# Kernel optimization log

Measured on AMD Instinct MI355X. Metric: run time of the kernel, lower is better.

The kernel has to match this reference:

```python
import jax, jax.numpy as jnp
import numpy as np

GDEP = 3      # number of diffusion steps
ALPHA = 0.05  # residual mixing coefficient


def setup_inputs() -> dict:
    key = jax.random.key(0)
    k1, k2, k3, k4 = jax.random.split(key, 4)
    B, C, N, L = 256, 32, 207, 12   # batch, channels, nodes, timesteps
    C_OUT = 32
    x = jax.random.normal(k1, (B, C, N, L), dtype=jnp.float32)
    adj = jax.random.uniform(k2, (N, N), dtype=jnp.float32)
    # mlp = 1x1 Conv2d(c_in, c_out): weight (c_out, c_in), bias (c_out,)
    W = jax.random.normal(k3, (C_OUT, C), dtype=jnp.float32) * 0.05
    b = jax.random.normal(k4, (C_OUT,), dtype=jnp.float32) * 0.05
    return {"x": x, "adj": adj, "W": W, "b": b}


def reference(x, adj, W, b):
    # Row-normalized adjacency with self loops: a = (adj + I) / rowsum
    N = adj.shape[0]
    a = adj + jnp.eye(N, dtype=adj.dtype)
    a = a / a.sum(axis=1, keepdims=True)
    # Iterative diffusion with alpha-residual mix
    h = x
    for _ in range(GDEP):
        # nconv: torch.einsum('ncwl,vw->ncvl', x, A)
        h = ALPHA * x + (1.0 - ALPHA) * jnp.einsum('ncwl,vw->ncvl', h, a)
    # mlp: 1x1 conv over channel dim + bias
    ho = jnp.einsum('ncvl,oc->novl', h, W) + b[None, :, None, None]
    return ho
```

## Files before the change

kernel.cpp:

```cpp
#include <hip/hip_runtime.h>

#define NN 207
#define ALPHA 0.05f
#define BETA  0.95f

typedef __attribute__((ext_vector_type(8))) short bf16x8;
typedef __attribute__((ext_vector_type(4))) float f32x4;

__device__ inline unsigned short f2bf(float f) {
    union { float f; unsigned int u; } v; v.f = f;
    unsigned int u = v.u;
    unsigned int r = (u + 0x7FFFu + ((u >> 16) & 1u)) >> 16;
    return (unsigned short)r;
}

__global__ __launch_bounds__(256) void k_norm(const float* __restrict__ adj,
                                              float* __restrict__ An,
                                              float* __restrict__ M1) {
    int v = blockIdx.x;
    int t = threadIdx.x;
    __shared__ float red[4];
    __shared__ float sinv;
    float s = 0.f;
    if (t < NN) s = adj[v * NN + t];
    s += __shfl_down(s, 32); s += __shfl_down(s, 16); s += __shfl_down(s, 8);
    s += __shfl_down(s, 4);  s += __shfl_down(s, 2);  s += __shfl_down(s, 1);
    if ((t & 63) == 0) red[t >> 6] = s;
    __syncthreads();
    if (t == 0) sinv = 1.0f / (red[0] + red[1] + red[2] + red[3] + 1.0f);
    __syncthreads();
    if (t < NN) {
        float val = (adj[v * NN + t] + (t == v ? 1.f : 0.f)) * sinv;
        An[v * NN + t] = val;
        M1[v * NN + t] = (t == v ? ALPHA : 0.f) + BETA * val;
    }
}

__global__ __launch_bounds__(256) void k_step(const float* __restrict__ A,
                                              const float* __restrict__ X,
                                              float* __restrict__ C) {
    __shared__ float As[32][68];
    __shared__ float Xs[32][68];
    const int t = threadIdx.x;
    const int bi = blockIdx.x;
    const int i0 = (bi >> 2) * 64, j0 = (bi & 3) * 64;
    const int ty = t >> 4, tx = t & 15;
    float acc[4][4] = {{0.f}};
    for (int kt = 0; kt < 7; ++kt) {
        __syncthreads();
        {
            int r = t >> 2, q = t & 3;
            int gi = i0 + r;
            #pragma unroll
            for (int h = 0; h < 2; ++h) {
                #pragma unroll
                for (int e = 0; e < 4; ++e) {
                    int u = kt * 32 + q * 8 + h * 4 + e;
                    float v = 0.f;
                    if (gi < NN && u < NN) v = A[gi * NN + u];
                    As[q * 8 + h * 4 + e][r] = v;
                }
            }
            int kk = t >> 3, p = t & 7;
            int gu = kt * 32 + kk;
            #pragma unroll
            for (int h = 0; h < 2; ++h) {
                #pragma unroll
                for (int e = 0; e < 4; ++e) {
                    int gj = j0 + p * 8 + h * 4 + e;
                    float v = 0.f;
                    if (gu < NN && gj < NN) v = X[gu * NN + gj];
                    Xs[kk][p * 8 + h * 4 + e] = v;
                }
            }
        }
        __syncthreads();
        #pragma unroll 8
        for (int kk = 0; kk < 32; ++kk) {
            float4 a = *(const float4*)&As[kk][ty * 4];
            float4 b = *(const float4*)&Xs[kk][tx * 4];
            const float* ap = &a.x; const float* bp = &b.x;
            #pragma unroll
            for (int ii = 0; ii < 4; ++ii)
                #pragma unroll
                for (int jj = 0; jj < 4; ++jj)
                    acc[ii][jj] = fmaf(ap[ii], bp[jj], acc[ii][jj]);
        }
    }
    #pragma unroll
    for (int ii = 0; ii < 4; ++ii) {
        int gi = i0 + ty * 4 + ii;
        if (gi < NN) {
            #pragma unroll
            for (int jj = 0; jj < 4; ++jj) {
                int gj = j0 + tx * 4 + jj;
                if (gj < NN)
                    C[gi * NN + gj] = (gi == gj ? ALPHA : 0.f) + BETA * acc[ii][jj];
            }
        }
    }
}

__global__ __launch_bounds__(64) void k_pack(const float* __restrict__ P,
                                             uint4* __restrict__ Pbf) {
    int g = blockIdx.x;
    int nt = g / 7, ks = g % 7;
    int lane = threadIdx.x;
    int v = nt * 16 + (lane & 15);
    int wb = ks * 32 + (lane >> 4) * 8;
    unsigned int d[4];
    #pragma unroll
    for (int p = 0; p < 4; ++p) {
        float lo = 0.f, hi = 0.f;
        int w = wb + 2 * p;
        if (v < NN) {
            if (w < NN)     lo = P[v * NN + w];
            if (w + 1 < NN) hi = P[v * NN + w + 1];
        }
        d[p] = (unsigned int)f2bf(lo) | ((unsigned int)f2bf(hi) << 16);
    }
    uint4 o; o.x = d[0]; o.y = d[1]; o.z = d[2]; o.w = d[3];
    Pbf[g * 64 + lane] = o;
}

__global__ __launch_bounds__(512) void k_main(const float* __restrict__ x,
                                              const uint4* __restrict__ Pbf,
                                              const float* __restrict__ Wm,
                                              const float* __restrict__ bias,
                                              float* __restrict__ out) {
    __shared__ __align__(16) char lds[52224];
    unsigned int* afrag = (unsigned int*)lds;
    float* ys = (float*)lds;

    const int n = blockIdx.x;
    const int t = threadIdx.x;
    const int lane = t & 63;
    const int wave = __builtin_amdgcn_readfirstlane(t >> 6);

    f32x4 acc[3][13];
    #pragma unroll
    for (int a = 0; a < 3; ++a)
        #pragma unroll
        for (int bI = 0; bI < 13; ++bI) acc[a][bI] = (f32x4)0.f;

    const float4* x4 = (const float4*)x;

    for (int ks = 0; ks < 7; ++ks) {
        __syncthreads();
        #pragma unroll
        for (int i = 0; i < 3; ++i) {
            int q = t + 512 * i;
            int c = q / 48, r = q % 48;
            int wp = r / 3, lseg = r % 3;
            int w0 = ks * 32 + 2 * wp;
            float4 va = make_float4(0.f, 0.f, 0.f, 0.f), vb = va;
            size_t base = (size_t)(n * 32 + c) * NN;
            if (w0 < NN)     va = x4[(base + w0) * 3 + lseg];
            if (w0 + 1 < NN) vb = x4[(base + w0 + 1) * 3 + lseg];
            int kblk = wp >> 2, dw = wp & 3;
            const float* vap = &va.x; const float* vbp = &vb.x;
            #pragma unroll
            for (int e = 0; e < 4; ++e) {
                int m = c * 12 + lseg * 4 + e;
                unsigned int pk = (unsigned int)f2bf(vap[e])
                                | ((unsigned int)f2bf(vbp[e]) << 16);
                afrag[(m >> 4) * 256 + ((m & 15) + 16 * kblk) * 4 + dw] = pk;
            }
        }
        __syncthreads();
        bf16x8 af[3];
        #pragma unroll
        for (int mt3 = 0; mt3 < 3; ++mt3)
            af[mt3] = ((const bf16x8*)lds)[(wave * 3 + mt3) * 64 + lane];
        #pragma unroll
        for (int nt = 0; nt < 13; ++nt) {
            uint4 braw = Pbf[(nt * 7 + ks) * 64 + lane];
            bf16x8 bf = __builtin_bit_cast(bf16x8, braw);
            #pragma unroll
            for (int mt3 = 0; mt3 < 3; ++mt3)
                acc[mt3][nt] = __builtin_amdgcn_mfma_f32_16x16x32_bf16(
                                   af[mt3], bf, acc[mt3][nt], 0, 0, 0);
        }
    }

    #pragma unroll
    for (int np = 0; np < 7; ++np) {
        __syncthreads();
        #pragma unroll
        for (int tl = 0; tl < 2; ++tl) {
            int nt = np * 2 + tl;
            if (nt < 13) {
                #pragma unroll
                for (int mt3 = 0; mt3 < 3; ++mt3) {
                    int mrow = (wave * 3 + mt3) * 16 + (lane >> 4) * 4;
                    #pragma unroll
                    for (int r = 0; r < 4; ++r)
                        ys[(mrow + r) * 34 + tl * 16 + (lane & 15)] = acc[mt3][nt][r];
                }
            }
        }
        __syncthreads();
        if (t < 384) {
            int tl = t / 192, rr = t % 192;
            int vv = rr / 12, l = rr % 12;
            int v = (np * 2 + tl) * 16 + vv;
            if (v < NN) {
                float y[32];
                #pragma unroll
                for (int c = 0; c < 32; ++c)
                    y[c] = ys[(c * 12 + l) * 34 + tl * 16 + vv];
                size_t ob = (size_t)n * 32 * (NN * 12) + (size_t)v * 12 + l;
                for (int o = 0; o < 32; ++o) {
                    float a = bias[o];
                    #pragma unroll
                    for (int c = 0; c < 32; ++c)
                        a = fmaf(Wm[o * 32 + c], y[c], a);
                    out[ob + (size_t)o * (NN * 12)] = a;
                }
            }
        }
    }
}

extern "C" void kernel_launch(void* const* d_in, const int* in_sizes, int n_in,
                              void* d_out, int out_size, void* d_ws, size_t ws_size,
                              hipStream_t stream) {
    const float* x   = (const float*)d_in[0];
    const float* adj = (const float*)d_in[1];
    const float* W   = (const float*)d_in[2];
    const float* b   = (const float*)d_in[3];
    float* out = (float*)d_out;
    float* ws  = (float*)d_ws;

    float* An  = ws;
    float* M1P = ws + 43008;
    float* M2  = ws + 86016;
    uint4* Pbf = (uint4*)ws;

    k_norm<<<NN, 256, 0, stream>>>(adj, An, M1P);
    k_step<<<16, 256, 0, stream>>>(An, M1P, M2);
    k_step<<<16, 256, 0, stream>>>(An, M2, M1P);
    k_pack<<<91, 64, 0, stream>>>(M1P, Pbf);
    k_main<<<256, 512, 0, stream>>>(x, Pbf, W, b, out);
}
```

Before: 261.4 us.

## Split main kernel across timestep segments, fuse bf16 packing into step kernel

The small adjacency power steps now run on 169 16x16 tiles instead of 16 blocks, and the bf16 packing pass is folded into the second step kernel, which removes one launch. The main kernel now uses 768 blocks, one per batch and 4-timestep segment, with an XCD-aware block-to-batch mapping. Each lane builds its MFMA A fragment straight from global memory, so the LDS staging and its barriers are gone. The catch is that x is reread with strided scalar loads and each block redoes the 1x1 conv epilogue for its own slice.

```diff
diff --git a/kernel.cpp b/kernel.cpp
--- a/kernel.cpp
+++ b/kernel.cpp
@@ -10,8 +10,7 @@
 __device__ inline unsigned short f2bf(float f) {
     union { float f; unsigned int u; } v; v.f = f;
     unsigned int u = v.u;
-    unsigned int r = (u + 0x7FFFu + ((u >> 16) & 1u)) >> 16;
-    return (unsigned short)r;
+    return (unsigned short)((u + 0x7FFFu + ((u >> 16) & 1u)) >> 16);
 }
 
 __global__ __launch_bounds__(256) void k_norm(const float* __restrict__ adj,
@@ -36,187 +35,169 @@
     }
 }
 
-__global__ __launch_bounds__(256) void k_step(const float* __restrict__ A,
-                                              const float* __restrict__ X,
-                                              float* __restrict__ C) {
-    __shared__ float As[32][68];
-    __shared__ float Xs[32][68];
+__global__ __launch_bounds__(256) void k_stepM(const float* __restrict__ A,
+                                               const float* __restrict__ X,
+                                               float* __restrict__ C) {
+    __shared__ float As[16 * 208];
+    __shared__ float Xs[16 * 212];
     const int t = threadIdx.x;
-    const int bi = blockIdx.x;
-    const int i0 = (bi >> 2) * 64, j0 = (bi & 3) * 64;
-    const int ty = t >> 4, tx = t & 15;
-    float acc[4][4] = {{0.f}};
-    for (int kt = 0; kt < 7; ++kt) {
-        __syncthreads();
-        {
-            int r = t >> 2, q = t & 3;
-            int gi = i0 + r;
-            #pragma unroll
-            for (int h = 0; h < 2; ++h) {
-                #pragma unroll
-                for (int e = 0; e < 4; ++e) {
-                    int u = kt * 32 + q * 8 + h * 4 + e;
-                    float v = 0.f;
-                    if (gi < NN && u < NN) v = A[gi * NN + u];
-                    As[q * 8 + h * 4 + e][r] = v;
-                }
-            }
-            int kk = t >> 3, p = t & 7;
-            int gu = kt * 32 + kk;
-            #pragma unroll
-            for (int h = 0; h < 2; ++h) {
-                #pragma unroll
-                for (int e = 0; e < 4; ++e) {
-                    int gj = j0 + p * 8 + h * 4 + e;
-                    float v = 0.f;
-                    if (gu < NN && gj < NN) v = X[gu * NN + gj];
-                    Xs[kk][p * 8 + h * 4 + e] = v;
-                }
-            }
-        }
-        __syncthreads();
-        #pragma unroll 8
-        for (int kk = 0; kk < 32; ++kk) {
-            float4 a = *(const float4*)&As[kk][ty * 4];
-            float4 b = *(const float4*)&Xs[kk][tx * 4];
-            const float* ap = &a.x; const float* bp = &b.x;
-            #pragma unroll
-            for (int ii = 0; ii < 4; ++ii)
-                #pragma unroll
-                for (int jj = 0; jj < 4; ++jj)
-                    acc[ii][jj] = fmaf(ap[ii], bp[jj], acc[ii][jj]);
-        }
-    }
-    #pragma unroll
-    for (int ii = 0; ii < 4; ++ii) {
-        int gi = i0 + ty * 4 + ii;
-        if (gi < NN) {
-            #pragma unroll
-            for (int jj = 0; jj < 4; ++jj) {
-                int gj = j0 + tx * 4 + jj;
-                if (gj < NN)
-                    C[gi * NN + gj] = (gi == gj ? ALPHA : 0.f) + BETA * acc[ii][jj];
-            }
-        }
-    }
-}
-
-__global__ __launch_bounds__(64) void k_pack(const float* __restrict__ P,
-                                             uint4* __restrict__ Pbf) {
-    int g = blockIdx.x;
-    int nt = g / 7, ks = g % 7;
-    int lane = threadIdx.x;
-    int v = nt * 16 + (lane & 15);
-    int wb = ks * 32 + (lane >> 4) * 8;
-    unsigned int d[4];
-    #pragma unroll
-    for (int p = 0; p < 4; ++p) {
-        float lo = 0.f, hi = 0.f;
-        int w = wb + 2 * p;
-        if (v < NN) {
-            if (w < NN)     lo = P[v * NN + w];
-            if (w + 1 < NN) hi = P[v * NN + w + 1];
-        }
-        d[p] = (unsigned int)f2bf(lo) | ((unsigned int)f2bf(hi) << 16);
-    }
-    uint4 o; o.x = d[0]; o.y = d[1]; o.z = d[2]; o.w = d[3];
-    Pbf[g * 64 + lane] = o;
-}
-
-__global__ __launch_bounds__(512) void k_main(const float* __restrict__ x,
-                                              const uint4* __restrict__ Pbf,
-                                              const float* __restrict__ Wm,
-                                              const float* __restrict__ bias,
-                                              float* __restrict__ out) {
-    __shared__ __align__(16) char lds[52224];
-    unsigned int* afrag = (unsigned int*)lds;
-    float* ys = (float*)lds;
-
-    const int n = blockIdx.x;
+    const int i0 = (blockIdx.x / 13) * 16, j0 = (blockIdx.x % 13) * 16;
+    const int r = t >> 4, cj = t & 15;
+    for (int p = 0; p < 13; ++p) {
+        int u = p * 16 + cj;
+        As[r * 208 + u] = (i0 + r < NN && u < NN) ? A[(i0 + r) * NN + u] : 0.f;
+        int u2 = p * 16 + r;
+        Xs[cj * 212 + u2] = (u2 < NN && j0 + cj < NN) ? X[u2 * NN + j0 + cj] : 0.f;
+    }
+    __syncthreads();
+    float s = 0.f;
+    for (int u = 0; u < 208; u += 4) {
+        float4 av = *(const float4*)&As[r * 208 + u];
+        float4 xv = *(const float4*)&Xs[cj * 212 + u];
+        s = fmaf(av.x, xv.x, s); s = fmaf(av.y, xv.y, s);
+        s = fmaf(av.z, xv.z, s); s = fmaf(av.w, xv.w, s);
+    }
+    int gi = i0 + r, gj = j0 + cj;
+    if (gi < NN && gj < NN)
+        C[gi * NN + gj] = (gi == gj ? ALPHA : 0.f) + BETA * s;
+}
+
+__global__ __launch_bounds__(256) void k_stepP(const float* __restrict__ A,
+                                               const float* __restrict__ X,
+                                               uint4* __restrict__ Pbf) {
+    __shared__ float As[16 * 208];
+    __shared__ float Xs[16 * 212];
+    __shared__ float Ct[16 * 17];
+    const int t = threadIdx.x;
+    const int nt = blockIdx.x / 13, jt = blockIdx.x % 13;
+    const int i0 = nt * 16, j0 = jt * 16;
+    const int r = t >> 4, cj = t & 15;
+    for (int p = 0; p < 13; ++p) {
+        int u = p * 16 + cj;
+        As[r * 208 + u] = (i0 + r < NN && u < NN) ? A[(i0 + r) * NN + u] : 0.f;
+        int u2 = p * 16 + r;
+        Xs[cj * 212 + u2] = (u2 < NN && j0 + cj < NN) ? X[u2 * NN + j0 + cj] : 0.f;
+    }
+    __syncthreads();
+    float s = 0.f;
+    for (int u = 0; u < 208; u += 4) {
+        float4 av = *(const float4*)&As[r * 208 + u];
+        float4 xv = *(const float4*)&Xs[cj * 212 + u];
+        s = fmaf(av.x, xv.x, s); s = fmaf(av.y, xv.y, s);
+        s = fmaf(av.z, xv.z, s); s = fmaf(av.w, xv.w, s);
+    }
+    int gi = i0 + r, gj = j0 + cj;
+    Ct[r * 17 + cj] = ((gi == gj && gi < NN) ? ALPHA : 0.f) + BETA * s;
+    __syncthreads();
+    if (t < 32) {
+        const int vv = t & 15, kb2 = t >> 4;
+        const int ks = jt >> 1;
+        const int kblk = (jt & 1) * 2 + kb2;
+        unsigned int d[4];
+        #pragma unroll
+        for (int p = 0; p < 4; ++p) {
+            float lo = Ct[vv * 17 + kb2 * 8 + 2 * p];
+            float hi = Ct[vv * 17 + kb2 * 8 + 2 * p + 1];
+            d[p] = (unsigned int)f2bf(lo) | ((unsigned int)f2bf(hi) << 16);
+        }
+        uint4 o; o.x = d[0]; o.y = d[1]; o.z = d[2]; o.w = d[3];
+        Pbf[(nt * 7 + ks) * 64 + vv + 16 * kblk] = o;
+        if (jt == 12) {
+            uint4 z; z.x = z.y = z.z = z.w = 0u;
+            Pbf[(nt * 7 + 6) * 64 + vv + 16 * (2 + kb2)] = z;
+        }
+    }
+}
+
+__global__ __launch_bounds__(512, 4) void k_main(const float* __restrict__ x,
+                                                 const uint4* __restrict__ Pbf,
+                                                 const float* __restrict__ Wm,
+                                                 const float* __restrict__ bias,
+                                                 float* __restrict__ out) {
+    __shared__ float ys[128 * 33];
+
+    const int b = blockIdx.x;
+    const int xcd = b & 7;
+    const int q = b >> 3;
+    const int lseg = q % 3;
+    const int n = (q / 3) * 8 + xcd;
+    const int l0 = lseg * 4;
+
     const int t = threadIdx.x;
     const int lane = t & 63;
     const int wave = __builtin_amdgcn_readfirstlane(t >> 6);
 
-    f32x4 acc[3][13];
+    const int c    = wave * 4 + ((lane >> 2) & 3);
+    const int dl   = lane & 3;
+    const int kblk = lane >> 4;
+    const float* xp = x + ((size_t)(n * 32 + c) * NN + kblk * 8) * 12 + l0 + dl;
+
+    f32x4 acc[13];
     #pragma unroll
-    for (int a = 0; a < 3; ++a)
-        #pragma unroll
-        for (int bI = 0; bI < 13; ++bI) acc[a][bI] = (f32x4)0.f;
-
-    const float4* x4 = (const float4*)x;
+    for (int i = 0; i < 13; ++i) acc[i] = (f32x4)0.f;
 
     for (int ks = 0; ks < 7; ++ks) {
-        __syncthreads();
-        #pragma unroll
-        for (int i = 0; i < 3; ++i) {
-            int q = t + 512 * i;
-            int c = q / 48, r = q % 48;
-            int wp = r / 3, lseg = r % 3;
-            int w0 = ks * 32 + 2 * wp;
-            float4 va = make_float4(0.f, 0.f, 0.f, 0.f), vb = va;
-            size_t base = (size_t)(n * 32 + c) * NN;
-            if (w0 < NN)     va = x4[(base + w0) * 3 + lseg];
-            if (w0 + 1 < NN) vb = x4[(base + w0 + 1) * 3 + lseg];
-            int kblk = wp >> 2, dw = wp & 3;
-            const float* vap = &va.x; const float* vbp = &vb.x;
-            #pragma unroll
-            for (int e = 0; e < 4; ++e) {
-                int m = c * 12 + lseg * 4 + e;
-                unsigned int pk = (unsigned int)f2bf(vap[e])
-                                | ((unsigned int)f2bf(vbp[e]) << 16);
-                afrag[(m >> 4) * 256 + ((m & 15) + 16 * kblk) * 4 + dw] = pk;
+        const float* xk = xp + ks * (32 * 12);
+        float xv[8];
+        if (ks < 6) {
+            #pragma unroll
+            for (int j = 0; j < 8; ++j) xv[j] = xk[j * 12];
+        } else {
+            #pragma unroll
+            for (int j = 0; j < 8; ++j) {
+                int w = 192 + kblk * 8 + j;
+                xv[j] = (w < NN) ? xk[j * 12] : 0.f;
             }
         }
-        __syncthreads();
-        bf16x8 af[3];
-        #pragma unroll
-        for (int mt3 = 0; mt3 < 3; ++mt3)
-            af[mt3] = ((const bf16x8*)lds)[(wave * 3 + mt3) * 64 + lane];
+        uint4 araw;
+        araw.x = (unsigned int)f2bf(xv[0]) | ((unsigned int)f2bf(xv[1]) << 16);
+        araw.y = (unsigned int)f2bf(xv[2]) | ((unsigned int)f2bf(xv[3]) << 16);
+        araw.z = (unsigned int)f2bf(xv[4]) | ((unsigned int)f2bf(xv[5]) << 16);
+        araw.w = (unsigned int)f2bf(xv[6]) | ((unsigned int)f2bf(xv[7]) << 16);
+        bf16x8 af = __builtin_bit_cast(bf16x8, araw);
+
+        const uint4* pb = Pbf + ks * 64 + lane;
         #pragma unroll
         for (int nt = 0; nt < 13; ++nt) {
-            uint4 braw = Pbf[(nt * 7 + ks) * 64 + lane];
-            bf16x8 bf = __builtin_bit_cast(bf16x8, braw);
-            #pragma unroll
-            for (int mt3 = 0; mt3 < 3; ++mt3)
-                acc[mt3][nt] = __builtin_amdgcn_mfma_f32_16x16x32_bf16(
-                                   af[mt3], bf, acc[mt3][nt], 0, 0, 0);
-        }
-    }
+            bf16x8 bfr = __builtin_bit_cast(bf16x8, pb[nt * 448]);
+            acc[nt] = __builtin_amdgcn_mfma_f32_16x16x32_bf16(af, bfr, acc[nt], 0, 0, 0);
+        }
+    }
+
+    const int s   = t & 127;
+    const int og  = __builtin_amdgcn_readfirstlane(t >> 7);
+    const int vloc = (s >> 2) & 15;
+    const int dlo  = s & 3;
+    const int ntl  = s >> 6;
 
     #pragma unroll
     for (int np = 0; np < 7; ++np) {
         __syncthreads();
         #pragma unroll
-        for (int tl = 0; tl < 2; ++tl) {
-            int nt = np * 2 + tl;
+        for (int ntw = 0; ntw < 2; ++ntw) {
+            int nt = np * 2 + ntw;
             if (nt < 13) {
                 #pragma unroll
-                for (int mt3 = 0; mt3 < 3; ++mt3) {
-                    int mrow = (wave * 3 + mt3) * 16 + (lane >> 4) * 4;
-                    #pragma unroll
-                    for (int r = 0; r < 4; ++r)
-                        ys[(mrow + r) * 34 + tl * 16 + (lane & 15)] = acc[mt3][nt][r];
-                }
+                for (int r = 0; r < 4; ++r)
+                    ys[(ntw * 64 + (lane & 15) * 4 + r) * 33 + wave * 4 + (lane >> 4)] = acc[nt][r];
             }
         }
         __syncthreads();
-        if (t < 384) {
-            int tl = t / 192, rr = t % 192;
-            int vv = rr / 12, l = rr % 12;
-            int v = (np * 2 + tl) * 16 + vv;
-            if (v < NN) {
-                float y[32];
+        int nt = np * 2 + ntl;
+        int v = nt * 16 + vloc;
+        if (nt < 13 && v < NN) {
+            float y[32];
+            #pragma unroll
+            for (int cc = 0; cc < 32; ++cc) y[cc] = ys[s * 33 + cc];
+            size_t ob = ((size_t)(n * 32) * NN + v) * 12 + l0 + dlo;
+            #pragma unroll
+            for (int oo = 0; oo < 8; ++oo) {
+                int o = og * 8 + oo;
+                float a = bias[o];
                 #pragma unroll
-                for (int c = 0; c < 32; ++c)
-                    y[c] = ys[(c * 12 + l) * 34 + tl * 16 + vv];
-                size_t ob = (size_t)n * 32 * (NN * 12) + (size_t)v * 12 + l;
-                for (int o = 0; o < 32; ++o) {
-                    float a = bias[o];
-                    #pragma unroll
-                    for (int c = 0; c < 32; ++c)
-                        a = fmaf(Wm[o * 32 + c], y[c], a);
-                    out[ob + (size_t)o * (NN * 12)] = a;
-                }
+                for (int cc = 0; cc < 32; ++cc)
+                    a = fmaf(Wm[o * 32 + cc], y[cc], a);
+                out[ob + (size_t)o * (NN * 12)] = a;
             }
         }
     }
@@ -233,13 +214,12 @@
     float* ws  = (float*)d_ws;
 
     float* An  = ws;
-    float* M1P = ws + 43008;
+    float* M1  = ws + 43008;
     float* M2  = ws + 86016;
-    uint4* Pbf = (uint4*)ws;
-
-    k_norm<<<NN, 256, 0, stream>>>(adj, An, M1P);
-    k_step<<<16, 256, 0, stream>>>(An, M1P, M2);
-    k_step<<<16, 256, 0, stream>>>(An, M2, M1P);
-    k_pack<<<91, 64, 0, stream>>>(M1P, Pbf);
-    k_main<<<256, 512, 0, stream>>>(x, Pbf, W, b, out);
-}
+    uint4* Pbf = (uint4*)(ws + 129024);
+
+    k_norm <<<NN, 256, 0, stream>>>(adj, An, M1);
+    k_stepM<<<169, 256, 0, stream>>>(An, M1, M2);
+    k_stepP<<<169, 256, 0, stream>>>(An, M2, Pbf);
+    k_main <<<768, 512, 0, stream>>>(x, Pbf, W, b, out);
+}
```

New measurement: 223.8 us. 14.4% less time.
